# Performance work log

Measured on AMD Instinct MI355X. Metric: run time of the kernel, lower is better.

The kernel has to match this reference:

```python
import jax, jax.numpy as jnp
import numpy as np

# edge types from metadata: (src_type, 'to', dst_type)
NODE_SRC = [0, 1, 2, 3, 0, 1, 2, 1, 3, 1]
NODE_DST = [0, 1, 2, 3, 1, 0, 1, 2, 1, 3]
N_NODES = 30000
N_EDGES = 400000
HEADS1 = 8


def _han_conv(xs, edges, proj_W, proj_b, att_src, att_dst, k_W, k_b, q, heads):
    """Faithful port of torch_geometric HANConv (eval mode, dropout off)."""
    out_ch = proj_W.shape[-1]
    D = out_ch // heads
    N = xs[0].shape[0]
    # per-node-type projection -> [N, H, D]
    h = [(xs[t] @ proj_W[t] + proj_b[t]).reshape(N, heads, D) for t in range(4)]
    outs = {t: [] for t in range(4)}
    for e in range(10):
        s, d = NODE_SRC[e], NODE_DST[e]
        row, col = edges[e, 0], edges[e, 1]
        a_src = (h[s] * att_src[e]).sum(-1)  # [N, H]
        a_dst = (h[d] * att_dst[e]).sum(-1)  # [N, H]
        alpha = jax.nn.leaky_relu(a_src[row] + a_dst[col], 0.2)  # [E, H]
        # segment softmax over incoming edges of each dst node
        amax = jax.ops.segment_max(alpha, col, num_segments=N)
        ex = jnp.exp(alpha - amax[col])
        denom = jax.ops.segment_sum(ex, col, num_segments=N)
        w = ex / (denom[col] + 1e-16)
        msg = h[s][row] * w[:, :, None]  # [E, H, D]
        agg = jax.ops.segment_sum(msg, col, num_segments=N).reshape(N, out_ch)
        outs[d].append(jax.nn.relu(agg))
    # semantic-level attention fusion across relations ending at each node type
    res = []
    for t in range(4):
        stk = jnp.stack(outs[t])  # [M, N, C]
        score = (q * jnp.tanh(stk @ k_W + k_b).mean(axis=1)).sum(-1)  # [M]
        sattn = jax.nn.softmax(score)
        res.append((sattn[:, None, None] * stk).sum(0))  # [N, C]
    return res


def setup_inputs() -> dict:
    key = jax.random.key(0)
    ks = jax.random.split(key, 24)
    inp = {}
    for t in range(4):
        inp[f"x{t}"] = jax.random.normal(ks[t], (N_NODES, 256), dtype=jnp.float32)
    inp["edges"] = jax.random.randint(ks[4], (10, 2, N_EDGES), 0, N_NODES, dtype=jnp.int32)
    s = 0.05
    inp["proj1_W"] = jax.random.normal(ks[5], (4, 256, 128), dtype=jnp.float32) * s
    inp["proj1_b"] = jax.random.normal(ks[6], (4, 128), dtype=jnp.float32) * s
    inp["att1_src"] = jax.random.normal(ks[7], (10, 8, 16), dtype=jnp.float32) * s
    inp["att1_dst"] = jax.random.normal(ks[8], (10, 8, 16), dtype=jnp.float32) * s
    inp["k1_W"] = jax.random.normal(ks[9], (128, 128), dtype=jnp.float32) * s
    inp["k1_b"] = jax.random.normal(ks[10], (128,), dtype=jnp.float32) * s
    inp["q1"] = jax.random.normal(ks[11], (128,), dtype=jnp.float32) * s
    inp["proj2_W"] = jax.random.normal(ks[12], (4, 128, 32), dtype=jnp.float32) * s
    inp["proj2_b"] = jax.random.normal(ks[13], (4, 32), dtype=jnp.float32) * s
    inp["att2_src"] = jax.random.normal(ks[14], (10, 1, 32), dtype=jnp.float32) * s
    inp["att2_dst"] = jax.random.normal(ks[15], (10, 1, 32), dtype=jnp.float32) * s
    inp["k2_W"] = jax.random.normal(ks[16], (32, 32), dtype=jnp.float32) * s
    inp["k2_b"] = jax.random.normal(ks[17], (32,), dtype=jnp.float32) * s
    inp["q2"] = jax.random.normal(ks[18], (32,), dtype=jnp.float32) * s
    return inp


def reference(x0, x1, x2, x3, edges,
              proj1_W, proj1_b, att1_src, att1_dst, k1_W, k1_b, q1,
              proj2_W, proj2_b, att2_src, att2_dst, k2_W, k2_b, q2):
    # eval mode: all F.dropout calls are identity
    xs = [x0, x1, x2, x3]
    h = _han_conv(xs, edges, proj1_W, proj1_b, att1_src, att1_dst, k1_W, k1_b, q1, HEADS1)
    h = [jax.nn.elu(v) for v in h]
    o = _han_conv(h, edges, proj2_W, proj2_b, att2_src, att2_dst, k2_W, k2_b, q2, 1)
    # final per-node softmax over channel dim for each node type; stack since all N equal
    return jnp.stack([jax.nn.softmax(v, axis=1) for v in o])  # [4, N, 32]
```

## Files before the change

kernel.cpp:

```cpp
#include <hip/hip_runtime.h>
#include <hip/hip_fp16.h>

#define NN 30000
#define NE 400000
#define NBUCK 59
#define BPR 98
#define EPB 4096
#define CAPREG 12288
#define BCAP 12288

__constant__ int d_SRC[10] = {0,1,2,3,0,1,2,1,3,1};
__constant__ int d_DST[10] = {0,1,2,3,1,0,1,2,1,3};
__constant__ int d_RORD[10] = {1,5,7,9,0,4,2,6,3,8};
__constant__ int d_GORD[10] = {0,4,1,5,7,9,2,6,3,8};
__constant__ int d_FCNT[4] = {2,4,2,2};
__constant__ int d_FREL[4][4] = {{0,5,0,0},{1,4,6,8},{2,7,0,0},{3,9,0,0}};

typedef _Float16 f16x8 __attribute__((ext_vector_type(8)));
typedef float f32x4 __attribute__((ext_vector_type(4)));

struct __attribute__((aligned(8))) h2x2 { __half2 a, b; };

template<int BN, bool AF16>
__global__ __launch_bounds__(256)
void mgemm_k(const float* __restrict__ A, long sA,
             const float* __restrict__ B, long sB,
             const float* __restrict__ bias, long sBias,
             float* __restrict__ C, long sC,
             int M, int K, int N, int relu_a, int epi)
{
    constexpr int BM = 128, BK = 32, MR = 2;
    constexpr int NF = BN / 16;
    constexpr int LDK = BK + 8;
    const int z = blockIdx.z;
    const _Float16* __restrict__ Ah = (const _Float16*)A;
    if constexpr (AF16) Ah += (long)z * sA; else A += (long)z * sA;
    B += (long)z * sB;
    bias += (long)z * sBias;
    C += (long)z * sC;
    const int m0 = blockIdx.x * BM;
    const int n0 = blockIdx.y * BN;
    const int tid = threadIdx.x;
    const int wv = tid >> 6;
    const int l  = tid & 63;
    const int fm = l & 15;
    const int fg = l >> 4;

    __shared__ _Float16 As[BM][LDK];
    __shared__ _Float16 Bs[BN][LDK];
    __shared__ float red[4][BN];

    f32x4 acc[MR][NF];
#pragma unroll
    for (int mr = 0; mr < MR; ++mr)
#pragma unroll
        for (int f = 0; f < NF; ++f) acc[mr][f] = (f32x4){0.f, 0.f, 0.f, 0.f};

    const int arow = tid >> 1;
    const int akc  = (tid & 1) << 4;
    const int grow = m0 + arow;

    for (int k0 = 0; k0 < K; k0 += BK) {
        f16x8 ap0, ap1;
        if (grow < M) {
            if constexpr (AF16) {
                const _Float16* aq = Ah + (long)grow * K + k0 + akc;
                ap0 = *(const f16x8*)aq;
                ap1 = *(const f16x8*)(aq + 8);
                if (relu_a) {
#pragma unroll
                    for (int j = 0; j < 8; ++j) {
                        ap0[j] = ap0[j] > (_Float16)0.f ? ap0[j] : (_Float16)0.f;
                        ap1[j] = ap1[j] > (_Float16)0.f ? ap1[j] : (_Float16)0.f;
                    }
                }
            } else {
                const float* aq = A + (long)grow * K + k0 + akc;
                float4 u0 = *(const float4*)aq;
                float4 u1 = *(const float4*)(aq + 4);
                float4 u2 = *(const float4*)(aq + 8);
                float4 u3 = *(const float4*)(aq + 12);
                float v[16] = {u0.x,u0.y,u0.z,u0.w, u1.x,u1.y,u1.z,u1.w,
                               u2.x,u2.y,u2.z,u2.w, u3.x,u3.y,u3.z,u3.w};
                if (relu_a) {
#pragma unroll
                    for (int j = 0; j < 16; ++j) v[j] = fmaxf(v[j], 0.f);
                }
#pragma unroll
                for (int j = 0; j < 8; ++j) { ap0[j] = (_Float16)v[j]; ap1[j] = (_Float16)v[j+8]; }
            }
        } else {
#pragma unroll
            for (int j = 0; j < 8; ++j) { ap0[j] = (_Float16)0.f; ap1[j] = (_Float16)0.f; }
        }
        *(f16x8*)&As[arow][akc]     = ap0;
        *(f16x8*)&As[arow][akc + 8] = ap1;

        if constexpr (BN == 64) {
            const int bk = tid >> 4;
            const int bn = (tid & 15) << 2;
#pragma unroll
            for (int kk = 0; kk < 2; ++kk) {
                int kr = bk + kk * 16;
                float4 u = *(const float4*)(B + (long)(k0 + kr) * N + n0 + bn);
                Bs[bn + 0][kr] = (_Float16)u.x;
                Bs[bn + 1][kr] = (_Float16)u.y;
                Bs[bn + 2][kr] = (_Float16)u.z;
                Bs[bn + 3][kr] = (_Float16)u.w;
            }
        } else {
            const int bk = tid >> 3;
            const int bn = (tid & 7) << 2;
            float4 u = *(const float4*)(B + (long)(k0 + bk) * N + n0 + bn);
            Bs[bn + 0][bk] = (_Float16)u.x;
            Bs[bn + 1][bk] = (_Float16)u.y;
            Bs[bn + 2][bk] = (_Float16)u.z;
            Bs[bn + 3][bk] = (_Float16)u.w;
        }
        __syncthreads();

        f16x8 a0 = *(const f16x8*)&As[wv * 32 + fm][fg * 8];
        f16x8 a1 = *(const f16x8*)&As[wv * 32 + 16 + fm][fg * 8];
#pragma unroll
        for (int f = 0; f < NF; ++f) {
            f16x8 b = *(const f16x8*)&Bs[f * 16 + fm][fg * 8];
            acc[0][f] = __builtin_amdgcn_mfma_f32_16x16x32_f16(a0, b, acc[0][f], 0, 0, 0);
            acc[1][f] = __builtin_amdgcn_mfma_f32_16x16x32_f16(a1, b, acc[1][f], 0, 0, 0);
        }
        __syncthreads();
    }

    if (epi == 0) {
#pragma unroll
        for (int f = 0; f < NF; ++f) {
            float bz = bias[n0 + f * 16 + fm];
#pragma unroll
            for (int mr = 0; mr < MR; ++mr)
#pragma unroll
                for (int i = 0; i < 4; ++i) {
                    int gr = m0 + wv * 32 + mr * 16 + fg * 4 + i;
                    if (gr < M) C[(long)gr * N + n0 + f * 16 + fm] = acc[mr][f][i] + bz;
                }
        }
    } else if (epi == 2) {
        __half* Ch = (__half*)C;
#pragma unroll
        for (int f = 0; f < NF; ++f) {
            float bz = bias[n0 + f * 16 + fm];
#pragma unroll
            for (int mr = 0; mr < MR; ++mr)
#pragma unroll
                for (int i = 0; i < 4; ++i) {
                    int gr = m0 + wv * 32 + mr * 16 + fg * 4 + i;
                    if (gr < M) Ch[(long)gr * N + n0 + f * 16 + fm] = __float2half(acc[mr][f][i] + bz);
                }
        }
    } else {
#pragma unroll
        for (int f = 0; f < NF; ++f) {
            float bz = bias[n0 + f * 16 + fm];
            float s = 0.f;
#pragma unroll
            for (int mr = 0; mr < MR; ++mr)
#pragma unroll
                for (int i = 0; i < 4; ++i) {
                    int gr = m0 + wv * 32 + mr * 16 + fg * 4 + i;
                    if (gr < M) s += tanhf(acc[mr][f][i] + bz);
                }
            s += __shfl_xor(s, 16, 64);
            s += __shfl_xor(s, 32, 64);
            if (fg == 0) red[wv][f * 16 + fm] = s;
        }
        __syncthreads();
        if (tid < BN) {
            float s = red[0][tid] + red[1][tid] + red[2][tid] + red[3][tid];
            unsafeAtomicAdd(&C[n0 + tid], s);
        }
    }
}

__global__ __launch_bounds__(256)
void init_bincur(int* __restrict__ binCur)
{
    int i = blockIdx.x * 256 + threadIdx.x;
    if (i < 10 * NBUCK) binCur[i] = (i % NBUCK) * CAPREG;
}

__global__ __launch_bounds__(256)
void csr_binA(const int* __restrict__ edges, int* __restrict__ binCur,
              unsigned* __restrict__ binned)
{
    __shared__ int lcnt[NBUCK];
    __shared__ int gbase[NBUCK];
    int rel = blockIdx.x / BPR;
    int blk = blockIdx.x - rel * BPR;
    int base = blk * EPB;
    int tid = threadIdx.x;
    for (int b = tid; b < NBUCK; b += 256) lcnt[b] = 0;
    __syncthreads();
    const int* er = edges + (long)rel * 2 * NE;
    const int* ec = er + NE;
    unsigned pk[16];
    unsigned mt[16];
#pragma unroll
    for (int k = 0; k < 16; ++k) {
        int i = base + k * 256 + tid;
        if (i < NE) {
            int r = er[i];
            int c = ec[i];
            int b = c >> 9;
            int lo = atomicAdd(&lcnt[b], 1);
            pk[k] = ((unsigned)c << 15) | (unsigned)r;
            mt[k] = ((unsigned)b << 16) | (unsigned)lo;
        } else {
            mt[k] = 0xFFFFFFFFu;
        }
    }
    __syncthreads();
    if (tid < NBUCK) gbase[tid] = atomicAdd(&binCur[rel * NBUCK + tid], lcnt[tid]);
    __syncthreads();
    unsigned* bn = binned + (long)rel * NBUCK * CAPREG;
#pragma unroll
    for (int k = 0; k < 16; ++k) {
        if (mt[k] != 0xFFFFFFFFu) {
            int b = mt[k] >> 16;
            int lo = mt[k] & 0xFFFF;
            bn[gbase[b] + lo] = pk[k];
        }
    }
}

__global__ __launch_bounds__(64)
void bucket_scan(const int* __restrict__ binCur, int* __restrict__ bbase,
                 int* __restrict__ off_all)
{
    int rel = blockIdx.x;
    int t = threadIdx.x;
    __shared__ int c[64];
    int v = (t < NBUCK) ? (binCur[rel * NBUCK + t] - t * CAPREG) : 0;
    c[t] = v;
    __syncthreads();
    for (int d = 1; d < 64; d <<= 1) {
        int u = (t >= d) ? c[t - d] : 0;
        __syncthreads();
        c[t] += u;
        __syncthreads();
    }
    if (t < NBUCK) bbase[rel * NBUCK + t] = c[t] - v;
    if (t == 0) off_all[rel * (NN + 1) + NN] = NE;
}

__global__ __launch_bounds__(256)
void csr_binB(const int* __restrict__ binCur, const int* __restrict__ bbase,
              const unsigned* __restrict__ binned,
              int* __restrict__ off_all, int* __restrict__ rows)
{
    __shared__ int cntS[512];
    __shared__ int lcur[512];
    __shared__ int part[256];
    __shared__ int buf[BCAP];
    int rel = blockIdx.x / NBUCK;
    int bkt = blockIdx.x - rel * NBUCK;
    const unsigned* bn = binned + ((long)rel * NBUCK + bkt) * CAPREG;
    int* off = off_all + rel * (NN + 1);
    int* rw = rows + (long)rel * NE;
    int cnt = binCur[rel * NBUCK + bkt] - bkt * CAPREG;
    int gbase = bbase[rel * NBUCK + bkt];
    int nb0 = bkt << 9;
    int nb1 = min(nb0 + 512, NN);
    int nloc = nb1 - nb0;
    int tid = threadIdx.x;

    cntS[tid] = 0; cntS[tid + 256] = 0;
    __syncthreads();
    for (int j = tid; j < cnt; j += 256) {
        int c = (int)(bn[j] >> 15);
        atomicAdd(&cntS[c - nb0], 1);
    }
    __syncthreads();
    int c0 = cntS[2 * tid], c1 = cntS[2 * tid + 1];
    part[tid] = c0 + c1;
    __syncthreads();
    for (int d = 1; d < 256; d <<= 1) {
        int u = (tid >= d) ? part[tid - d] : 0;
        __syncthreads();
        part[tid] += u;
        __syncthreads();
    }
    int pre = (tid == 0) ? 0 : part[tid - 1];
    cntS[2 * tid] = pre;
    cntS[2 * tid + 1] = pre + c0;
    __syncthreads();
    for (int i = tid; i < nloc; i += 256) off[nb0 + i] = gbase + cntS[i];
    lcur[tid] = cntS[tid]; lcur[tid + 256] = cntS[tid + 256];
    __syncthreads();
    if (cnt <= BCAP) {
        for (int j = tid; j < cnt; j += 256) {
            unsigned p = bn[j];
            int r = (int)(p & 0x7FFF);
            int c = (int)(p >> 15);
            int pos = atomicAdd(&lcur[c - nb0], 1);
            buf[pos] = r;
        }
        __syncthreads();
        for (int i = tid; i < cnt; i += 256) rw[gbase + i] = buf[i];
    } else {
        for (int j = tid; j < cnt; j += 256) {
            unsigned p = bn[j];
            int r = (int)(p & 0x7FFF);
            int c = (int)(p >> 15);
            int pos = atomicAdd(&lcur[c - nb0], 1);
            rw[gbase + pos] = r;
        }
    }
}

__global__ __launch_bounds__(256)
void attn_dots1(const __half* __restrict__ h1h,
                const float* __restrict__ att_src,
                const float* __restrict__ att_dst,
                float* __restrict__ asrc, float* __restrict__ adst)
{
    int gid = blockIdx.x * 256 + threadIdx.x;
    int wave = gid >> 6;
    int lane = gid & 63;
    if (wave >= 4 * NN) return;
    int t = wave / NN;
    int n = wave - t * NN;
    __half2 hh = *(const __half2*)&h1h[(long)(t * NN + n) * 128 + 2 * lane];
    float2 hv = __half22float2(hh);
    const int SRCc[10] = {0,1,2,3,0,1,2,1,3,1};
    const int DSTc[10] = {0,1,2,3,1,0,1,2,1,3};
#pragma unroll
    for (int e = 0; e < 10; ++e) {
        if (SRCc[e] == t) {
            float2 av = *(const float2*)&att_src[e * 128 + 2 * lane];
            float p = hv.x * av.x + hv.y * av.y;
#pragma unroll
            for (int off = 1; off < 8; off <<= 1) p += __shfl_xor(p, off, 64);
            if ((lane & 7) == 0) asrc[(long)(e * NN + n) * 8 + (lane >> 3)] = p;
        }
        if (DSTc[e] == t) {
            float2 bv = *(const float2*)&att_dst[e * 128 + 2 * lane];
            float p = hv.x * bv.x + hv.y * bv.y;
#pragma unroll
            for (int off = 1; off < 8; off <<= 1) p += __shfl_xor(p, off, 64);
            if ((lane & 7) == 0) adst[(long)(e * NN + n) * 8 + (lane >> 3)] = p;
        }
    }
}

__global__ __launch_bounds__(256)
void gather_agg1_all(const int* __restrict__ csr_off, const int* __restrict__ csr_rows,
                     const float* __restrict__ asrc1, const float* __restrict__ adst1,
                     const __half* __restrict__ h1h, __half* __restrict__ slots16)
{
    int e = d_GORD[blockIdx.y];
    int node = blockIdx.x * 4 + (threadIdx.x >> 6);
    int lane = threadIdx.x & 63;
    if (node >= NN) return;
    const int* off = csr_off + e * (NN + 1);
    const int* rows = csr_rows + (long)e * NE;
    const float* asrc_e = asrc1 + (long)e * NN * 8;
    const float* adst_e = adst1 + (long)e * NN * 8;
    const _Float16* h1s = (const _Float16*)h1h + (long)d_SRC[e] * NN * 128;
    __half* out = slots16 + (long)e * NN * 128;

    const int g2  = lane >> 4;
    const int s16 = lane & 15;
    const int hv  = s16 >> 1;
    const int eA  = lane >> 3;
    const int hA  = lane & 7;
    int beg = off[node], end = off[node + 1];
    float adA = adst_e[node * 8 + hA];
    float den = (g2 == 0) ? 1e-16f : 0.f;
    float a0 = 0.f, a1 = 0.f, a2 = 0.f, a3 = 0.f;
    float a4 = 0.f, a5 = 0.f, a6 = 0.f, a7 = 0.f;

#define GA1_STEP(i)                                                              \
    {                                                                            \
        int e0 = 4 * (i) + g2;                                                   \
        float wi = __shfl(w, e0 * 8 + hv, 64);                                   \
        int ri = __shfl(r, e0 * 8, 64);                                          \
        f16x8 v = *(const f16x8*)(h1s + (long)ri * 128 + 8 * s16);               \
        den += wi;                                                               \
        a0 += wi * (float)v[0]; a1 += wi * (float)v[1];                          \
        a2 += wi * (float)v[2]; a3 += wi * (float)v[3];                          \
        a4 += wi * (float)v[4]; a5 += wi * (float)v[5];                          \
        a6 += wi * (float)v[6]; a7 += wi * (float)v[7];                          \
    }

    if (beg < end) {
        int j0 = beg;
        int jj = j0 + eA;
        bool ok = jj < end;
        int r = rows[ok ? jj : beg];
        float aw = asrc_e[r * 8 + hA] + adA;
        while (true) {
            float al = aw > 0.f ? aw : 0.2f * aw;
            float w = ok ? __expf(al) : 0.f;
            int j1 = j0 + 8;
            int rn = r; float awn = 0.f; bool okn = false;
            if (j1 < end) {
                int jn = j1 + eA;
                okn = jn < end;
                rn = rows[okn ? jn : beg];
                awn = asrc_e[rn * 8 + hA] + adA;
            }
            int cnt = end - j0;
            GA1_STEP(0)
            if (cnt > 4) { GA1_STEP(1) }
            if (j1 >= end) break;
            j0 = j1; r = rn; aw = awn; ok = okn;
        }
    }
#undef GA1_STEP
#pragma unroll
    for (int m = 16; m < 64; m <<= 1) {
        a0 += __shfl_xor(a0, m, 64); a1 += __shfl_xor(a1, m, 64);
        a2 += __shfl_xor(a2, m, 64); a3 += __shfl_xor(a3, m, 64);
        a4 += __shfl_xor(a4, m, 64); a5 += __shfl_xor(a5, m, 64);
        a6 += __shfl_xor(a6, m, 64); a7 += __shfl_xor(a7, m, 64);
        den += __shfl_xor(den, m, 64);
    }
    if (g2 == 0) {
        float inv = 1.0f / den;
        f16x8 o;
        o[0] = (_Float16)(a0 * inv); o[1] = (_Float16)(a1 * inv);
        o[2] = (_Float16)(a2 * inv); o[3] = (_Float16)(a3 * inv);
        o[4] = (_Float16)(a4 * inv); o[5] = (_Float16)(a5 * inv);
        o[6] = (_Float16)(a6 * inv); o[7] = (_Float16)(a7 * inv);
        *(f16x8*)((_Float16*)out + (long)node * 128 + 8 * s16) = o;
    }
}

__global__ __launch_bounds__(256)
void fusion_all(const __half* __restrict__ slots16, const float* __restrict__ sattn,
                __half* __restrict__ h1f)
{
    int t = blockIdx.y;
    int idx = blockIdx.x * 256 + threadIdx.x;
    if (idx >= NN * 32) return;
    int c4 = idx & 31;
    int n = idx >> 5;
    long off = (long)n * 128 + c4 * 4;
    int cnt = d_FCNT[t];
    float o0 = 0.f, o1 = 0.f, o2 = 0.f, o3 = 0.f;
    for (int j = 0; j < cnt; ++j) {
        int e = d_FREL[t][j];
        float w = sattn[e];
        const __half* p = slots16 + (long)e * NN * 128 + off;
        float2 v01 = __half22float2(*(const __half2*)p);
        float2 v23 = __half22float2(*(const __half2*)(p + 2));
        o0 += w * fmaxf(v01.x, 0.f);
        o1 += w * fmaxf(v01.y, 0.f);
        o2 += w * fmaxf(v23.x, 0.f);
        o3 += w * fmaxf(v23.y, 0.f);
    }
    o0 = o0 > 0.f ? o0 : __expf(o0) - 1.f;
    o1 = o1 > 0.f ? o1 : __expf(o1) - 1.f;
    o2 = o2 > 0.f ? o2 : __expf(o2) - 1.f;
    o3 = o3 > 0.f ? o3 : __expf(o3) - 1.f;
    __half* q = h1f + (long)t * NN * 128 + off;
    *(__half2*)q = __floats2half2_rn(o0, o1);
    *(__half2*)(q + 2) = __floats2half2_rn(o2, o3);
}

__global__ __launch_bounds__(256)
void attn_dots2(const __half* __restrict__ h2h,
                const float* __restrict__ att_src,
                const float* __restrict__ att_dst,
                float* __restrict__ asrc, float* __restrict__ adst)
{
    int gid = blockIdx.x * 256 + threadIdx.x;
    int p = gid >> 5;
    int l = gid & 31;
    if (p >= 10 * NN) return;
    int e = p / NN, n = p - e * NN;
    int s = d_SRC[e], d = d_DST[e];
    float hs = __half2float(h2h[(long)(s * NN + n) * 32 + l]);
    float hd = __half2float(h2h[(long)(d * NN + n) * 32 + l]);
    float ps = hs * att_src[e * 32 + l];
    float pd = hd * att_dst[e * 32 + l];
#pragma unroll
    for (int off = 1; off < 32; off <<= 1) {
        ps += __shfl_xor(ps, off, 64);
        pd += __shfl_xor(pd, off, 64);
    }
    if (l == 0) { asrc[e * NN + n] = ps; adst[e * NN + n] = pd; }
}

__global__ __launch_bounds__(256)
void gather_agg2(const int* __restrict__ csr_off, const int* __restrict__ csr_rows,
                 const __half* __restrict__ h2h,
                 const float* __restrict__ asrc, const float* __restrict__ adst,
                 __half* __restrict__ agg2h)
{
    int e = d_RORD[blockIdx.y];
    int node = blockIdx.x * 8 + (threadIdx.x >> 5);
    int lane = threadIdx.x & 31;
    if (node >= NN) return;
    const int* off = csr_off + e * (NN + 1);
    const int* rows = csr_rows + (long)e * NE;
    const __half* h2s = h2h + (long)d_SRC[e] * NN * 32;
    const float* as = asrc + e * NN;
    const int slot = lane >> 3;
    const int sub = lane & 7;
    float ad = adst[e * NN + node];
    int beg = off[node], end = off[node + 1];
    float den = (slot == 0) ? 1e-16f : 0.f;
    float a0 = 0.f, a1 = 0.f, a2 = 0.f, a3 = 0.f;

#define GA2_STEP(i)                                                              \
    {                                                                            \
        int e0 = (i) * 4 + slot;                                                 \
        float wi = __shfl(w, e0, 32);                                            \
        int ri = __shfl(r, e0, 32);                                              \
        h2x2 v = *(const h2x2*)(h2s + (long)ri * 32 + 4 * sub);                  \
        float2 f0 = __half22float2(v.a);                                         \
        float2 f1 = __half22float2(v.b);                                         \
        den += wi;                                                               \
        a0 += wi * f0.x; a1 += wi * f0.y; a2 += wi * f1.x; a3 += wi * f1.y;      \
    }

    for (int j0 = beg; j0 < end; j0 += 32) {
        int jj = j0 + lane;
        bool ok = jj < end;
        int r = rows[ok ? jj : beg];
        float a = as[r] + ad;
        a = a > 0.f ? a : 0.2f * a;
        float w = ok ? __expf(a) : 0.f;
        int cnt = end - j0;
        if (cnt >= 32) {
            GA2_STEP(0) GA2_STEP(1) GA2_STEP(2) GA2_STEP(3)
            GA2_STEP(4) GA2_STEP(5) GA2_STEP(6) GA2_STEP(7)
        } else {
            int it = (cnt + 3) >> 2;
            for (int i = 0; i < it; ++i) GA2_STEP(i)
        }
    }
#undef GA2_STEP
#pragma unroll
    for (int m = 8; m < 32; m <<= 1) {
        a0 += __shfl_xor(a0, m, 32);
        a1 += __shfl_xor(a1, m, 32);
        a2 += __shfl_xor(a2, m, 32);
        a3 += __shfl_xor(a3, m, 32);
        den += __shfl_xor(den, m, 32);
    }
    if (slot == 0) {
        float inv = 1.0f / den;
        h2x2 o;
        o.a = __floats2half2_rn(a0 * inv, a1 * inv);
        o.b = __floats2half2_rn(a2 * inv, a3 * inv);
        *(h2x2*)(agg2h + ((long)e * NN + node) * 32 + 4 * sub) = o;
    }
}

__global__ void score_all_k(const float* __restrict__ colsum, const float* __restrict__ q,
                            float* __restrict__ sattn, int C)
{
    __shared__ float sc[10];
    int tid = threadIdx.x;
    if (tid < 10) {
        float s = 0.f;
        for (int c = 0; c < C; ++c) s += q[c] * colsum[tid * C + c];
        sc[tid] = s / (float)NN;
    }
    __syncthreads();
    if (tid < 4) {
        float mx = -1e30f;
        for (int m = 0; m < 10; ++m) if (d_DST[m] == tid) mx = fmaxf(mx, sc[m]);
        float ex[10];
        float sum = 0.f;
        for (int m = 0; m < 10; ++m) {
            ex[m] = 0.f;
            if (d_DST[m] == tid) { ex[m] = __expf(sc[m] - mx); sum += ex[m]; }
        }
        for (int m = 0; m < 10; ++m) if (d_DST[m] == tid) sattn[m] = ex[m] / sum;
    }
}

__global__ __launch_bounds__(256)
void final_softmax(const __half* __restrict__ agg, const float* __restrict__ sattn,
                   float* __restrict__ out)
{
    int gid = blockIdx.x * 256 + threadIdx.x;
    int c = gid & 31;
    int p = gid >> 5;
    if (p >= 4 * NN) return;
    int t = p / NN, n = p - t * NN;
    float f = 0.f;
    for (int m = 0; m < 10; ++m) {
        if (d_DST[m] != t) continue;
        f += sattn[m] * fmaxf(__half2float(agg[(long)(m * NN + n) * 32 + c]), 0.f);
    }
    float mx = f;
#pragma unroll
    for (int off = 1; off < 32; off <<= 1) mx = fmaxf(mx, __shfl_xor(mx, off, 64));
    float ex = __expf(f - mx);
    float sm = ex;
#pragma unroll
    for (int off = 1; off < 32; off <<= 1) sm += __shfl_xor(sm, off, 64);
    out[(long)(t * NN + n) * 32 + c] = ex / sm;
}

extern "C" void kernel_launch(void* const* d_in, const int* in_sizes, int n_in,
                              void* d_out, int out_size, void* d_ws, size_t ws_size,
                              hipStream_t stream) {
    const float* x[4] = {
        (const float*)d_in[0], (const float*)d_in[1],
        (const float*)d_in[2], (const float*)d_in[3]};
    const int* edges = (const int*)d_in[4];
    const float* W1    = (const float*)d_in[5];
    const float* b1    = (const float*)d_in[6];
    const float* att1s = (const float*)d_in[7];
    const float* att1d = (const float*)d_in[8];
    const float* k1W   = (const float*)d_in[9];
    const float* k1b   = (const float*)d_in[10];
    const float* q1    = (const float*)d_in[11];
    const float* W2    = (const float*)d_in[12];
    const float* b2    = (const float*)d_in[13];
    const float* att2s = (const float*)d_in[14];
    const float* att2d = (const float*)d_in[15];
    const float* k2W   = (const float*)d_in[16];
    const float* k2b   = (const float*)d_in[17];
    const float* q2    = (const float*)d_in[18];

    float* W = (float*)d_ws;
    __half* h1h    = (__half*)W;
    __half* h1f    = (__half*)W;
    __half* h2h    = (__half*)(W + 7680000);
    __half* slots16 = (__half*)(W + 15360000);
    __half* agg2h  = (__half*)(W + 15360000);
    unsigned* binned = (unsigned*)(W + 15360000);
    int*   binCur  = (int*)(W + 15360000 + 7249920);
    int*   bbase   = binCur + 640;
    float* asrc1   = W + 34560000;
    float* adst1   = W + 36960000;
    float* asrc2   = W + 36960000;
    float* adst2   = W + 37260000;
    float* colsum1 = W + 39360000;
    float* sattn1  = W + 39361280;
    float* colsum2 = W + 39361296;
    float* sattn2  = W + 39361616;
    int*   csr_off = (int*)(W + 39361640);
    int*   csr_row = csr_off + 300016;

    init_bincur<<<3, 256, 0, stream>>>(binCur);
    csr_binA<<<BPR * 10, 256, 0, stream>>>(edges, binCur, binned);
    bucket_scan<<<10, 64, 0, stream>>>(binCur, bbase, csr_off);
    csr_binB<<<NBUCK * 10, 256, 0, stream>>>(binCur, bbase, binned, csr_off, csr_row);

    hipMemsetAsync(colsum1, 0, 1632L * 4, stream);

    for (int t = 0; t < 4; ++t) {
        mgemm_k<64, false><<<dim3(235, 2, 1), 256, 0, stream>>>(
            x[t], 0, W1 + (long)t * 256 * 128, 0, b1 + t * 128, 0,
            (float*)(h1h + (long)t * NN * 128), 0, NN, 256, 128, 0, 2);
    }

    attn_dots1<<<30000, 256, 0, stream>>>(h1h, att1s, att1d, asrc1, adst1);

    gather_agg1_all<<<dim3(7500, 10), 256, 0, stream>>>(
        csr_off, csr_row, asrc1, adst1, h1h, slots16);

    mgemm_k<64, true><<<dim3(235, 2, 10), 256, 0, stream>>>(
        (const float*)slots16, (long)NN * 128, k1W, 0, k1b, 0,
        colsum1, 128, NN, 128, 128, 1, 1);
    score_all_k<<<1, 64, 0, stream>>>(colsum1, q1, sattn1, 128);

    fusion_all<<<dim3(3750, 4), 256, 0, stream>>>(slots16, sattn1, h1f);

    mgemm_k<32, true><<<dim3(235, 1, 4), 256, 0, stream>>>(
        (const float*)h1f, (long)NN * 128, W2, 128L * 32, b2, 32,
        (float*)h2h, (long)NN * 16, NN, 128, 32, 0, 2);

    attn_dots2<<<37500, 256, 0, stream>>>(h2h, att2s, att2d, asrc2, adst2);
    gather_agg2<<<dim3(3750, 10), 256, 0, stream>>>(
        csr_off, csr_row, h2h, asrc2, adst2, agg2h);

    mgemm_k<32, true><<<dim3(235, 1, 10), 256, 0, stream>>>(
        (const float*)agg2h, (long)NN * 32, k2W, 0, k2b, 0,
        colsum2, 32L, NN, 32, 32, 1, 1);
    score_all_k<<<1, 64, 0, stream>>>(colsum2, q2, sattn2, 32);
    final_softmax<<<15000, 256, 0, stream>>>(agg2h, sattn2, (float*)d_out);
}
```

Baseline: 761.2 us.

## Pin gather relations to XCDs and store CSR row indices as 16-bit

The layer-1 gather now uses a flat 1D grid. Each block index is mapped so that blocks landing on the same XCD (block id mod 8) process relations that share a source node type, which is meant to improve L2 reuse of the gathered h1 rows on MI355X's per-XCD L2 caches. CSR row indices are also narrowed from int32 to uint16, since node ids fit in 15 bits, halving index traffic in both gather kernels. This relies on the hardware's round-robin assignment of blocks to XCDs and on hand-computed tables for the relation split.

```diff
diff --git a/kernel.cpp b/kernel.cpp
--- a/kernel.cpp
+++ b/kernel.cpp
@@ -12,9 +12,13 @@
 __constant__ int d_SRC[10] = {0,1,2,3,0,1,2,1,3,1};
 __constant__ int d_DST[10] = {0,1,2,3,1,0,1,2,1,3};
 __constant__ int d_RORD[10] = {1,5,7,9,0,4,2,6,3,8};
-__constant__ int d_GORD[10] = {0,4,1,5,7,9,2,6,3,8};
 __constant__ int d_FCNT[4] = {2,4,2,2};
 __constant__ int d_FREL[4][4] = {{0,5,0,0},{1,4,6,8},{2,7,0,0},{3,9,0,0}};
+
+__constant__ int d_XRELA[8]  = {0,4,2,6,8,1,5,7};
+__constant__ int d_XBASEA[8] = {0,1875,3750,5625,0,1875,3750,5625};
+__constant__ int d_XCNTA[8]  = {7500,5625,3750,1875,7500,5625,3750,1875};
+__constant__ int d_XRELB[8]  = {4,2,6,3,1,5,7,9};
 
 typedef _Float16 f16x8 __attribute__((ext_vector_type(8)));
 typedef float f32x4 __attribute__((ext_vector_type(4)));
@@ -253,7 +257,7 @@
 __global__ __launch_bounds__(256)
 void csr_binB(const int* __restrict__ binCur, const int* __restrict__ bbase,
               const unsigned* __restrict__ binned,
-              int* __restrict__ off_all, int* __restrict__ rows)
+              int* __restrict__ off_all, unsigned short* __restrict__ rows)
 {
     __shared__ int cntS[512];
     __shared__ int lcur[512];
@@ -263,7 +267,7 @@
     int bkt = blockIdx.x - rel * NBUCK;
     const unsigned* bn = binned + ((long)rel * NBUCK + bkt) * CAPREG;
     int* off = off_all + rel * (NN + 1);
-    int* rw = rows + (long)rel * NE;
+    unsigned short* rw = rows + (long)rel * NE;
     int cnt = binCur[rel * NBUCK + bkt] - bkt * CAPREG;
     int gbase = bbase[rel * NBUCK + bkt];
     int nb0 = bkt << 9;
@@ -303,14 +307,14 @@
             buf[pos] = r;
         }
         __syncthreads();
-        for (int i = tid; i < cnt; i += 256) rw[gbase + i] = buf[i];
+        for (int i = tid; i < cnt; i += 256) rw[gbase + i] = (unsigned short)buf[i];
     } else {
         for (int j = tid; j < cnt; j += 256) {
             unsigned p = bn[j];
             int r = (int)(p & 0x7FFF);
             int c = (int)(p >> 15);
             int pos = atomicAdd(&lcur[c - nb0], 1);
-            rw[gbase + pos] = r;
+            rw[gbase + pos] = (unsigned short)r;
         }
     }
 }
@@ -351,16 +355,22 @@
 }
 
 __global__ __launch_bounds__(256)
-void gather_agg1_all(const int* __restrict__ csr_off, const int* __restrict__ csr_rows,
+void gather_agg1_all(const int* __restrict__ csr_off,
+                     const unsigned short* __restrict__ csr_rows,
                      const float* __restrict__ asrc1, const float* __restrict__ adst1,
                      const __half* __restrict__ h1h, __half* __restrict__ slots16)
 {
-    int e = d_GORD[blockIdx.y];
-    int node = blockIdx.x * 4 + (threadIdx.x >> 6);
+    int g = blockIdx.x;
+    int xcd = g & 7;
+    int slot = g >> 3;
+    int e, i;
+    if (slot < d_XCNTA[xcd]) { e = d_XRELA[xcd]; i = d_XBASEA[xcd] + slot; }
+    else                     { e = d_XRELB[xcd]; i = slot - d_XCNTA[xcd]; }
+    int node = i * 4 + (threadIdx.x >> 6);
     int lane = threadIdx.x & 63;
     if (node >= NN) return;
     const int* off = csr_off + e * (NN + 1);
-    const int* rows = csr_rows + (long)e * NE;
+    const unsigned short* rows = csr_rows + (long)e * NE;
     const float* asrc_e = asrc1 + (long)e * NN * 8;
     const float* adst_e = adst1 + (long)e * NN * 8;
     const _Float16* h1s = (const _Float16*)h1h + (long)d_SRC[e] * NN * 128;
@@ -394,7 +404,7 @@
         int j0 = beg;
         int jj = j0 + eA;
         bool ok = jj < end;
-        int r = rows[ok ? jj : beg];
+        int r = (int)rows[ok ? jj : beg];
         float aw = asrc_e[r * 8 + hA] + adA;
         while (true) {
             float al = aw > 0.f ? aw : 0.2f * aw;
@@ -404,7 +414,7 @@
             if (j1 < end) {
                 int jn = j1 + eA;
                 okn = jn < end;
-                rn = rows[okn ? jn : beg];
+                rn = (int)rows[okn ? jn : beg];
                 awn = asrc_e[rn * 8 + hA] + adA;
             }
             int cnt = end - j0;
@@ -491,7 +501,8 @@
 }
 
 __global__ __launch_bounds__(256)
-void gather_agg2(const int* __restrict__ csr_off, const int* __restrict__ csr_rows,
+void gather_agg2(const int* __restrict__ csr_off,
+                 const unsigned short* __restrict__ csr_rows,
                  const __half* __restrict__ h2h,
                  const float* __restrict__ asrc, const float* __restrict__ adst,
                  __half* __restrict__ agg2h)
@@ -501,7 +512,7 @@
     int lane = threadIdx.x & 31;
     if (node >= NN) return;
     const int* off = csr_off + e * (NN + 1);
-    const int* rows = csr_rows + (long)e * NE;
+    const unsigned short* rows = csr_rows + (long)e * NE;
     const __half* h2s = h2h + (long)d_SRC[e] * NN * 32;
     const float* as = asrc + e * NN;
     const int slot = lane >> 3;
@@ -526,7 +537,7 @@
     for (int j0 = beg; j0 < end; j0 += 32) {
         int jj = j0 + lane;
         bool ok = jj < end;
-        int r = rows[ok ? jj : beg];
+        int r = (int)rows[ok ? jj : beg];
         float a = as[r] + ad;
         a = a > 0.f ? a : 0.2f * a;
         float w = ok ? __expf(a) : 0.f;
@@ -645,7 +656,7 @@
     float* colsum2 = W + 39361296;
     float* sattn2  = W + 39361616;
     int*   csr_off = (int*)(W + 39361640);
-    int*   csr_row = csr_off + 300016;
+    unsigned short* csr_row = (unsigned short*)(csr_off + 300016);
 
     init_bincur<<<3, 256, 0, stream>>>(binCur);
     csr_binA<<<BPR * 10, 256, 0, stream>>>(edges, binCur, binned);
@@ -662,7 +673,7 @@
 
     attn_dots1<<<30000, 256, 0, stream>>>(h1h, att1s, att1d, asrc1, adst1);
 
-    gather_agg1_all<<<dim3(7500, 10), 256, 0, stream>>>(
+    gather_agg1_all<<<75000, 256, 0, stream>>>(
         csr_off, csr_row, asrc1, adst1, h1h, slots16);
 
     mgemm_k<64, true><<<dim3(235, 2, 10), 256, 0, stream>>>(
```

Result: no change. 762.3 us (+0.1%).
